# Kernel tuning notes

Hardware: AMD Instinct MI355X
Metric: run time of the kernel (lower is better)

## Reference

```python
import jax, jax.numpy as jnp
import numpy as np

B, S, D, H = 2, 2048, 2048, 16
HD = D // H            # 128
HALF = HD // 2         # 64
SOFTCAP = 50.0
ROPE_BASE = 10000.0


def setup_inputs() -> dict:
    key = jax.random.key(0)
    k1, k2, k3 = jax.random.split(key, 3)
    inputs = jax.random.normal(k1, (B, S, D), dtype=jnp.float32)
    # param init ~ nnx.initializers.normal() (stddev 0.01 default; scale to keep activations sane)
    w_in = jax.random.normal(k2, (D, H, 3 * HD), dtype=jnp.float32) * (1.0 / np.sqrt(D))
    w_out = jax.random.normal(k3, (H, HD, D), dtype=jnp.float32) * (1.0 / np.sqrt(D))
    # RoPE tables: [S, HALF]
    pos = jnp.arange(S, dtype=jnp.float32)[:, None]
    inv_freq = 1.0 / (ROPE_BASE ** (jnp.arange(HALF, dtype=jnp.float32) / HALF))
    ang = pos * inv_freq[None, :]
    rope_sin = jnp.sin(ang)
    rope_cos = jnp.cos(ang)
    # causal mask [1, 1, S, S]
    mask = jnp.tril(jnp.ones((S, S), dtype=bool))[None, None, :, :]
    return {"inputs": inputs, "w_in": w_in, "w_out": w_out,
            "rope_sin": rope_sin, "rope_cos": rope_cos, "mask": mask}


def apply_rope(x, sin, cos):
    # x: [B, S, H, HD]; sin/cos: [S, HALF] -> broadcast [1, S, 1, HALF]
    sin = sin[None, :, None, :]
    cos = cos[None, :, None, :]
    x1, x2 = x[..., :HALF], x[..., HALF:]
    return jnp.concatenate([x1 * cos - x2 * sin, x2 * cos + x1 * sin], axis=-1)


def reference(inputs, w_in, w_out, rope_sin, rope_cos, mask):
    dtype = inputs.dtype
    # fused QKV projection: [B, S, H, 3*HD]
    qkv = jnp.einsum('bsd,bhf->bshf'.replace('bhf', 'dhf'), inputs, w_in)
    q, k, v = jnp.split(qkv, 3, axis=-1)           # each [B, S, H, HD]
    q = apply_rope(q, rope_sin, rope_cos)
    k = apply_rope(k, rope_sin, rope_cos)
    q = q / jnp.sqrt(jnp.asarray(HD, dtype))
    scores = jnp.einsum('bqhd,bkhd->bhqk', q, k)   # [B, H, S, S]
    big_neg = jnp.finfo(dtype).min
    scores = jnp.where(mask, scores, big_neg)
    scores = jnp.tanh(scores / SOFTCAP) * SOFTCAP  # softcap
    attn = jax.nn.softmax(scores, axis=-1)
    x = jnp.einsum('bhqk,bkhd->bqhd', attn, v)     # [B, S, H, HD]
    out = jnp.einsum('bqhd,hdm->bqm', x, w_out)    # [B, S, D]
    return out
```

## Files before the change

### kernel.cpp

```cpp
#include <hip/hip_runtime.h>

#define B_ 2
#define S_ 2048
#define D_ 2048
#define H_ 16
#define HD_ 128
#define NT_ (S_ / 64)

typedef unsigned short u16;
typedef __bf16 bf16x8 __attribute__((ext_vector_type(8)));
typedef float f32x4 __attribute__((ext_vector_type(4)));

__device__ __forceinline__ float bf2f(u16 u) {
  unsigned int x = ((unsigned int)u) << 16;
  return __builtin_bit_cast(float, x);
}
__device__ __forceinline__ u16 f2bf(float f) {
  unsigned int u = __builtin_bit_cast(unsigned int, f);
  u += 0x7fffu + ((u >> 16) & 1u);
  return (u16)(u >> 16);
}
__device__ __forceinline__ void async16(const void* g, void* l) {
  __builtin_amdgcn_global_load_lds((const __attribute__((address_space(1))) void*)g,
                                   (__attribute__((address_space(3))) void*)l, 16, 0, 0);
}
__device__ __forceinline__ float vexp2(float x) {
  float r;
  asm("v_exp_f32 %0, %1" : "=v"(r) : "v"(x));
  return r;
}
__device__ __forceinline__ float vrcp(float x) {
  float r;
  asm("v_rcp_f32 %0, %1" : "=v"(r) : "v"(x));
  return r;
}

__global__ __launch_bounds__(256) void conv_f32_bf16(const float* __restrict__ in,
                                                     u16* __restrict__ outp, int n) {
  int idx = (blockIdx.x * 256 + threadIdx.x) * 4;
  int stride = gridDim.x * 256 * 4;
  for (; idx < n; idx += stride) {
    float4 v = *(const float4*)(in + idx);
    ushort4 ov = make_ushort4(f2bf(v.x), f2bf(v.y), f2bf(v.z), f2bf(v.w));
    *(ushort4*)(outp + idx) = ov;
  }
}

__global__ __launch_bounds__(256) void transpose_conv(const float* __restrict__ in,
                                                      u16* __restrict__ outp, int R, int C) {
  __shared__ float tile[32][33];
  int c0 = blockIdx.x * 32, r0 = blockIdx.y * 32;
  int tx = threadIdx.x & 31, ty = threadIdx.x >> 5;
#pragma unroll
  for (int yy = 0; yy < 32; yy += 8)
    tile[ty + yy][tx] = in[(size_t)(r0 + ty + yy) * C + c0 + tx];
  __syncthreads();
#pragma unroll
  for (int yy = 0; yy < 32; yy += 8)
    outp[(size_t)(c0 + ty + yy) * R + r0 + tx] = f2bf(tile[tx][ty + yy]);
}

__global__ __launch_bounds__(256) void transpose_v(const u16* __restrict__ in,
                                                   u16* __restrict__ outp) {
  __shared__ u16 tile[32][33];
  int bhh = blockIdx.z;
  const u16* ip = in + (size_t)bhh * S_ * HD_;
  u16* op = outp + (size_t)bhh * HD_ * S_;
  int hd0 = blockIdx.x * 32, s0 = blockIdx.y * 32;
  int tx = threadIdx.x & 31, ty = threadIdx.x >> 5;
#pragma unroll
  for (int yy = 0; yy < 32; yy += 8)
    tile[ty + yy][tx] = ip[(size_t)(s0 + ty + yy) * HD_ + hd0 + tx];
  __syncthreads();
#pragma unroll
  for (int yy = 0; yy < 32; yy += 8)
    op[(size_t)(hd0 + ty + yy) * S_ + s0 + tx] = tile[tx][ty + yy];
}

__global__ __launch_bounds__(256) void rope_kernel(u16* __restrict__ Q, u16* __restrict__ Kk,
                                                   const float* __restrict__ rsin,
                                                   const float* __restrict__ rcos) {
  int t = blockIdx.x * 256 + threadIdx.x;
  u16* base = blockIdx.y ? Kk : Q;
  float scale = blockIdx.y ? 1.0f : 0.08838834764831845f;
  int row = t >> 3, seg = t & 7;
  int s = row & (S_ - 1);
  int i0 = seg * 8;
  u16* p = base + (size_t)row * HD_;
  alignas(16) u16 x1[8], x2[8], o1[8], o2[8];
  *(uint4*)x1 = *(const uint4*)(p + i0);
  *(uint4*)x2 = *(const uint4*)(p + 64 + i0);
  alignas(16) float sn[8], cs[8];
  *(float4*)sn = *(const float4*)(rsin + s * 64 + i0);
  *(float4*)(sn + 4) = *(const float4*)(rsin + s * 64 + i0 + 4);
  *(float4*)cs = *(const float4*)(rcos + s * 64 + i0);
  *(float4*)(cs + 4) = *(const float4*)(rcos + s * 64 + i0 + 4);
#pragma unroll
  for (int j = 0; j < 8; ++j) {
    float a = bf2f(x1[j]), bb = bf2f(x2[j]);
    o1[j] = f2bf((a * cs[j] - bb * sn[j]) * scale);
    o2[j] = f2bf((bb * cs[j] + a * sn[j]) * scale);
  }
  *(uint4*)(p + i0) = *(uint4*)o1;
  *(uint4*)(p + 64 + i0) = *(uint4*)o2;
}

template <int EPI>
__global__ __launch_bounds__(256) void gemm_bt(const u16* __restrict__ A, const u16* __restrict__ Bt,
                                               float* __restrict__ C, int M, int N, int K,
                                               u16* __restrict__ Qo, u16* __restrict__ Ko,
                                               u16* __restrict__ Vo) {
  __shared__ alignas(16) u16 lsA[128 * 32];
  __shared__ alignas(16) u16 lsB[128 * 32];
  const int tid = threadIdx.x;
  const int lane = tid & 63, wid = tid >> 6;
  const int g = lane >> 4, lr = lane & 15;
  const int wr = wid >> 1, wc = wid & 1;
  const int m0 = blockIdx.y * 128, n0 = blockIdx.x * 128;
  f32x4 acc[4][4] = {};
  const int nk = K >> 5;
  for (int kt = 0; kt < nk; ++kt) {
    const int k0 = kt << 5;
    __syncthreads();
#pragma unroll
    for (int p = 0; p < 2; ++p) {
      const int c = p * 256 + tid;
      const int row = c >> 2;
      const int wb = (c & 3) << 4;
      async16((const char*)(A + (size_t)(m0 + row) * K + k0) + wb, (char*)lsA + c * 16);
      async16((const char*)(Bt + (size_t)(n0 + row) * K + k0) + wb, (char*)lsB + c * 16);
    }
    __syncthreads();
    bf16x8 af[4], bfr[4];
#pragma unroll
    for (int i = 0; i < 4; ++i)
      af[i] = *(const bf16x8*)((const char*)lsA + (wr * 64 + i * 16 + lr) * 64 + g * 16);
#pragma unroll
    for (int j = 0; j < 4; ++j)
      bfr[j] = *(const bf16x8*)((const char*)lsB + (wc * 64 + j * 16 + lr) * 64 + g * 16);
#pragma unroll
    for (int i = 0; i < 4; ++i)
#pragma unroll
      for (int j = 0; j < 4; ++j)
        acc[i][j] = __builtin_amdgcn_mfma_f32_16x16x32_bf16(af[i], bfr[j], acc[i][j], 0, 0, 0);
  }
  if (EPI == 0) {
#pragma unroll
    for (int i = 0; i < 4; ++i)
#pragma unroll
      for (int j = 0; j < 4; ++j)
#pragma unroll
        for (int r = 0; r < 4; ++r) {
          int m = m0 + wr * 64 + i * 16 + 4 * g + r;
          int n = n0 + wc * 64 + j * 16 + lr;
          C[(size_t)m * N + n] = acc[i][j][r];
        }
  } else {
    const int t = blockIdx.x;
    const int part = t % 3, h = t / 3;
    u16* dst = (part == 0) ? Qo : (part == 1 ? Ko : Vo);
#pragma unroll
    for (int i = 0; i < 4; ++i)
#pragma unroll
      for (int j = 0; j < 4; ++j)
#pragma unroll
        for (int r = 0; r < 4; ++r) {
          int m = m0 + wr * 64 + i * 16 + 4 * g + r;
          int hd = wc * 64 + j * 16 + lr;
          int b = m >> 11, s = m & (S_ - 1);
          dst[((size_t)(b * H_ + h) * S_ + s) * HD_ + hd] = f2bf(acc[i][j][r]);
        }
  }
}

__global__ __launch_bounds__(256) void attn_fwd(const u16* __restrict__ Q, const u16* __restrict__ K,
                                                const u16* __restrict__ VT, u16* __restrict__ X) {
  const int bx = blockIdx.x;
  const int bh = blockIdx.y;
  const int tid = threadIdx.x;
  const int lane = tid & 63, wid = tid >> 6;
  const int g = lane >> 4, lr = lane & 15;

  __shared__ alignas(16) u16 lsK[2][64 * 128];
  __shared__ alignas(16) u16 lsV[2][128 * 64];
  __shared__ alignas(16) u16 lsP[4][16 * 72];

  const u16* Qp = Q + (size_t)bh * S_ * HD_;
  const u16* Kp = K + (size_t)bh * S_ * HD_;
  const u16* Vp = VT + (size_t)bh * HD_ * S_;
  u16* myP = lsP[wid];
  const int b = bh >> 4, h = bh & 15;

  const float c1 = -0.057707802f;
  const float c2 = -144.26950409f;

#pragma unroll 1
  for (int pass = 0; pass < 2; ++pass) {
    const int qt = pass ? bx : (NT_ - 1 - bx);
    const int qrow = qt * 64 + wid * 16 + lr;
    const int qbase = qt * 64 + wid * 16 + 4 * g;

    bf16x8 qf[4];
#pragma unroll
    for (int kc = 0; kc < 4; ++kc)
      qf[kc] = *(const bf16x8*)(Qp + (size_t)qrow * HD_ + kc * 32 + g * 8);

    f32x4 o[8] = {};
    float psum[4] = {0.f, 0.f, 0.f, 0.f};

#pragma unroll
    for (int p = 0; p < 4; ++p) {
      int c = p * 256 + tid;
      int rowk = c >> 4;
      int wsk = ((c & 15) << 4) ^ ((rowk & 7) << 4);
      async16((const char*)Kp + (((size_t)rowk) << 8) + wsk, (char*)lsK[0] + c * 16);
      int rowv = c >> 3;
      int wsv = ((c & 7) << 4) ^ ((rowv & 7) << 4);
      async16((const char*)Vp + (size_t)rowv * (S_ * 2) + wsv, (char*)lsV[0] + c * 16);
    }
    __syncthreads();

    int cur = 0;
    for (int kt = 0; kt <= qt; ++kt) {
      if (kt < qt) {
        const int nxt = kt + 1;
#pragma unroll
        for (int p = 0; p < 4; ++p) {
          int c = p * 256 + tid;
          int rowk = c >> 4;
          int wsk = ((c & 15) << 4) ^ ((rowk & 7) << 4);
          async16((const char*)Kp + (((size_t)(nxt * 64 + rowk)) << 8) + wsk,
                  (char*)lsK[cur ^ 1] + c * 16);
          int rowv = c >> 3;
          int wsv = ((c & 7) << 4) ^ ((rowv & 7) << 4);
          async16((const char*)Vp + (size_t)rowv * (S_ * 2) + nxt * 128 + wsv,
                  (char*)lsV[cur ^ 1] + c * 16);
        }
      }
      f32x4 sc[4];
#pragma unroll
      for (int jn = 0; jn < 4; ++jn) {
        f32x4 a = {0.f, 0.f, 0.f, 0.f};
        const int row = jn * 16 + lr;
        const int sw = (row & 7) << 4;
#pragma unroll
        for (int kc = 0; kc < 4; ++kc) {
          int w = (kc * 64 + g * 16) ^ sw;
          bf16x8 kf = *(const bf16x8*)((const char*)lsK[cur] + row * 256 + w);
          a = __builtin_amdgcn_mfma_f32_16x16x32_bf16(qf[kc], kf, a, 0, 0, 0);
        }
        sc[jn] = a;
      }
#pragma unroll
      for (int jn = 0; jn < 4; ++jn) {
        int key = kt * 64 + jn * 16 + lr;
#pragma unroll
        for (int r = 0; r < 4; ++r) {
          float z = vexp2(c1 * sc[jn][r]);
          float p = vexp2(c2 * z * vrcp(1.f + z));
          if (key > qbase + r) p = 0.f;
          psum[r] += p;
          myP[(4 * g + r) * 72 + jn * 16 + lr] = f2bf(p);
        }
      }
#pragma unroll
      for (int kc = 0; kc < 2; ++kc) {
        bf16x8 pa = *(const bf16x8*)(myP + lr * 72 + kc * 32 + g * 8);
#pragma unroll
        for (int jh = 0; jh < 8; ++jh) {
          int row = jh * 16 + lr;
          int w = (kc * 64 + g * 16) ^ ((row & 7) << 4);
          bf16x8 vf = *(const bf16x8*)((const char*)lsV[cur] + row * 128 + w);
          o[jh] = __builtin_amdgcn_mfma_f32_16x16x32_bf16(pa, vf, o[jh], 0, 0, 0);
        }
      }
      __syncthreads();
      cur ^= 1;
    }
    float lsum[4];
#pragma unroll
    for (int r = 0; r < 4; ++r) {
      float s = psum[r];
#pragma unroll
      for (int msk = 1; msk < 16; msk <<= 1) s += __shfl_xor(s, msk, 64);
      lsum[r] = s;
    }
#pragma unroll
    for (int r = 0; r < 4; ++r) {
      float inv = 1.f / lsum[r];
      int s = qbase + r;
      u16* xp = X + ((size_t)(b * S_ + s)) * D_ + h * HD_;
#pragma unroll
      for (int jh = 0; jh < 8; ++jh) xp[jh * 16 + lr] = f2bf(o[jh][r] * inv);
    }
  }
}

extern "C" void kernel_launch(void* const* d_in, const int* in_sizes, int n_in,
                              void* d_out, int out_size, void* d_ws, size_t ws_size,
                              hipStream_t stream) {
  const float* inputs = (const float*)d_in[0];
  const float* w_in = (const float*)d_in[1];
  const float* w_out = (const float*)d_in[2];
  const float* rsin = (const float*)d_in[3];
  const float* rcos = (const float*)d_in[4];
  float* out = (float*)d_out;

  char* ws = (char*)d_ws;
  u16* bfA = (u16*)(ws);
  u16* w_inT = (u16*)(ws + 16777216);
  u16* Qraw = (u16*)(ws + 41943040);
  u16* Kraw = (u16*)(ws + 58720256);
  u16* Vraw = (u16*)(ws + 75497472);
  u16* VT = (u16*)(ws + 92274688);
  u16* Xbuf = (u16*)(ws);
  u16* w_outT = (u16*)(ws + 16777216);

  conv_f32_bf16<<<2048, 256, 0, stream>>>(inputs, bfA, B_ * S_ * D_);
  transpose_conv<<<dim3(6144 / 32, 2048 / 32), 256, 0, stream>>>(w_in, w_inT, 2048, 6144);
  gemm_bt<1><<<dim3(48, 32), 256, 0, stream>>>(bfA, w_inT, nullptr, 4096, 6144, 2048,
                                               Qraw, Kraw, Vraw);
  transpose_conv<<<dim3(2048 / 32, 2048 / 32), 256, 0, stream>>>(w_out, w_outT, 2048, 2048);
  rope_kernel<<<dim3(2048, 2), 256, 0, stream>>>(Qraw, Kraw, rsin, rcos);
  transpose_v<<<dim3(4, 64, 32), 256, 0, stream>>>(Vraw, VT);
  attn_fwd<<<dim3(NT_ / 2, 32), 256, 0, stream>>>(Qraw, Kraw, VT, Xbuf);
  gemm_bt<0><<<dim3(16, 32), 256, 0, stream>>>(Xbuf, w_outT, out, 4096, 2048, 2048,
                                               nullptr, nullptr, nullptr);
}
```

Measured before the change: 319.5 us.

## Rewrite GEMM with 6-stage async LDS pipeline, swizzled LDS, 256x128 tiles

Replaces the single-buffered 128x128 GEMM with a 512-thread 256x128 tile kernel. It keeps five K-tiles in flight through a six-buffer ring of async global-to-LDS loads, with XOR-swizzled LDS addressing to avoid bank conflicts. It also remaps workgroups with a grid swizzle for cache locality and raises wave priority around the MFMA block. The goal is to hide global load latency that the old per-iteration double sync exposed. In exchange it uses much more LDS (about 147KB), which caps occupancy at one block per CU, and it relies on a hand-set vmcnt wait.

```diff
diff --git a/kernel.cpp b/kernel.cpp
--- a/kernel.cpp
+++ b/kernel.cpp
@@ -6,6 +6,7 @@
 #define H_ 16
 #define HD_ 128
 #define NT_ (S_ / 64)
+#define NBUF 6
 
 typedef unsigned short u16;
 typedef __bf16 bf16x8 __attribute__((ext_vector_type(8)));
@@ -106,44 +107,83 @@
 }
 
 template <int EPI>
-__global__ __launch_bounds__(256) void gemm_bt(const u16* __restrict__ A, const u16* __restrict__ Bt,
-                                               float* __restrict__ C, int M, int N, int K,
-                                               u16* __restrict__ Qo, u16* __restrict__ Ko,
-                                               u16* __restrict__ Vo) {
-  __shared__ alignas(16) u16 lsA[128 * 32];
-  __shared__ alignas(16) u16 lsB[128 * 32];
+__global__ __launch_bounds__(512, 1) void gemm8p(const u16* __restrict__ A,
+                                                 const u16* __restrict__ Bt,
+                                                 float* __restrict__ C, int K, int N, int gx,
+                                                 u16* __restrict__ Qo, u16* __restrict__ Ko,
+                                                 u16* __restrict__ Vo) {
+  __shared__ alignas(16) u16 lsA[NBUF][256 * 32];
+  __shared__ alignas(16) u16 lsB[NBUF][128 * 32];
   const int tid = threadIdx.x;
-  const int lane = tid & 63, wid = tid >> 6;
+  const int lane = tid & 63;
+  const int wid = tid >> 6;
   const int g = lane >> 4, lr = lane & 15;
-  const int wr = wid >> 1, wc = wid & 1;
-  const int m0 = blockIdx.y * 128, n0 = blockIdx.x * 128;
+  const int wm = wid >> 1, wn = wid & 1;
+
+  const int nwg = gx << 4;
+  const int bid = blockIdx.x;
+  const int swz = (bid & 7) * (nwg >> 3) + (bid >> 3);
+  const int m_idx = swz & 15, n_idx = swz >> 4;
+  const size_t m0 = (size_t)m_idx * 256, n0 = (size_t)n_idx * 128;
+
+  const int la0 = tid, la1 = 512 + tid;
+  const int rowA0 = la0 >> 2, slA0 = la0 & 3;
+  const int rowA1 = la1 >> 2, slA1 = la1 & 3;
+  const int rowB = tid >> 2, slB = tid & 3;
+  const u16* srcA0 = A + (m0 + rowA0) * K + ((slA0 ^ ((rowA0 >> 1) & 3)) << 3);
+  const u16* srcA1 = A + (m0 + rowA1) * K + ((slA1 ^ ((rowA1 >> 1) & 3)) << 3);
+  const u16* srcB = Bt + (n0 + rowB) * K + ((slB ^ ((rowB >> 1) & 3)) << 3);
+
+#define STAGE(t, bufi)                                          \
+  {                                                             \
+    const int koff = (t) << 5;                                  \
+    async16(srcA0 + koff, (char*)lsA[bufi] + la0 * 16);         \
+    async16(srcA1 + koff, (char*)lsA[bufi] + la1 * 16);         \
+    async16(srcB + koff, (char*)lsB[bufi] + tid * 16);          \
+  }
+
+  int ofsA[4], ofsB[4];
+#pragma unroll
+  for (int i = 0; i < 4; ++i) {
+    int ra = wm * 64 + i * 16 + lr;
+    ofsA[i] = ra * 64 + ((g ^ ((ra >> 1) & 3)) << 4);
+    int rb = wn * 64 + i * 16 + lr;
+    ofsB[i] = rb * 64 + ((g ^ ((rb >> 1) & 3)) << 4);
+  }
+
   f32x4 acc[4][4] = {};
   const int nk = K >> 5;
+
+#pragma unroll
+  for (int t = 0; t < NBUF - 1; ++t) STAGE(t, t);
+  asm volatile("s_waitcnt vmcnt(12)" ::: "memory");
+  __builtin_amdgcn_s_barrier();
+
+  int buf = 0;
+#pragma unroll 1
   for (int kt = 0; kt < nk; ++kt) {
-    const int k0 = kt << 5;
-    __syncthreads();
-#pragma unroll
-    for (int p = 0; p < 2; ++p) {
-      const int c = p * 256 + tid;
-      const int row = c >> 2;
-      const int wb = (c & 3) << 4;
-      async16((const char*)(A + (size_t)(m0 + row) * K + k0) + wb, (char*)lsA + c * 16);
-      async16((const char*)(Bt + (size_t)(n0 + row) * K + k0) + wb, (char*)lsB + c * 16);
-    }
-    __syncthreads();
     bf16x8 af[4], bfr[4];
 #pragma unroll
-    for (int i = 0; i < 4; ++i)
-      af[i] = *(const bf16x8*)((const char*)lsA + (wr * 64 + i * 16 + lr) * 64 + g * 16);
-#pragma unroll
-    for (int j = 0; j < 4; ++j)
-      bfr[j] = *(const bf16x8*)((const char*)lsB + (wc * 64 + j * 16 + lr) * 64 + g * 16);
+    for (int i = 0; i < 4; ++i) af[i] = *(const bf16x8*)((const char*)lsA[buf] + ofsA[i]);
+#pragma unroll
+    for (int j = 0; j < 4; ++j) bfr[j] = *(const bf16x8*)((const char*)lsB[buf] + ofsB[j]);
+    const int st = kt + NBUF - 1;
+    const int sbuf = buf == 0 ? NBUF - 1 : buf - 1;
+    if (st < nk) STAGE(st, sbuf);
+    __builtin_amdgcn_s_barrier();
+    __builtin_amdgcn_s_setprio(1);
 #pragma unroll
     for (int i = 0; i < 4; ++i)
 #pragma unroll
       for (int j = 0; j < 4; ++j)
         acc[i][j] = __builtin_amdgcn_mfma_f32_16x16x32_bf16(af[i], bfr[j], acc[i][j], 0, 0, 0);
-  }
+    __builtin_amdgcn_s_setprio(0);
+    asm volatile("s_waitcnt vmcnt(12)" ::: "memory");
+    __builtin_amdgcn_s_barrier();
+    buf = buf == NBUF - 1 ? 0 : buf + 1;
+  }
+#undef STAGE
+
   if (EPI == 0) {
 #pragma unroll
     for (int i = 0; i < 4; ++i)
@@ -151,13 +191,12 @@
       for (int j = 0; j < 4; ++j)
 #pragma unroll
         for (int r = 0; r < 4; ++r) {
-          int m = m0 + wr * 64 + i * 16 + 4 * g + r;
-          int n = n0 + wc * 64 + j * 16 + lr;
-          C[(size_t)m * N + n] = acc[i][j][r];
+          size_t m = m0 + wm * 64 + i * 16 + 4 * g + r;
+          size_t n = n0 + wn * 64 + j * 16 + lr;
+          C[m * N + n] = acc[i][j][r];
         }
   } else {
-    const int t = blockIdx.x;
-    const int part = t % 3, h = t / 3;
+    const int part = n_idx % 3, h = n_idx / 3;
     u16* dst = (part == 0) ? Qo : (part == 1 ? Ko : Vo);
 #pragma unroll
     for (int i = 0; i < 4; ++i)
@@ -165,8 +204,8 @@
       for (int j = 0; j < 4; ++j)
 #pragma unroll
         for (int r = 0; r < 4; ++r) {
-          int m = m0 + wr * 64 + i * 16 + 4 * g + r;
-          int hd = wc * 64 + j * 16 + lr;
+          int m = (int)m0 + wm * 64 + i * 16 + 4 * g + r;
+          int hd = wn * 64 + j * 16 + lr;
           int b = m >> 11, s = m & (S_ - 1);
           dst[((size_t)(b * H_ + h) * S_ + s) * HD_ + hd] = f2bf(acc[i][j][r]);
         }
@@ -318,12 +357,11 @@
 
   conv_f32_bf16<<<2048, 256, 0, stream>>>(inputs, bfA, B_ * S_ * D_);
   transpose_conv<<<dim3(6144 / 32, 2048 / 32), 256, 0, stream>>>(w_in, w_inT, 2048, 6144);
-  gemm_bt<1><<<dim3(48, 32), 256, 0, stream>>>(bfA, w_inT, nullptr, 4096, 6144, 2048,
-                                               Qraw, Kraw, Vraw);
+  gemm8p<1><<<768, 512, 0, stream>>>(bfA, w_inT, nullptr, 2048, 6144, 48, Qraw, Kraw, Vraw);
   transpose_conv<<<dim3(2048 / 32, 2048 / 32), 256, 0, stream>>>(w_out, w_outT, 2048, 2048);
   rope_kernel<<<dim3(2048, 2), 256, 0, stream>>>(Qraw, Kraw, rsin, rcos);
   transpose_v<<<dim3(4, 64, 32), 256, 0, stream>>>(Vraw, VT);
   attn_fwd<<<dim3(NT_ / 2, 32), 256, 0, stream>>>(Qraw, Kraw, VT, Xbuf);
-  gemm_bt<0><<<dim3(16, 32), 256, 0, stream>>>(Xbuf, w_outT, out, 4096, 2048, 2048,
-                                               nullptr, nullptr, nullptr);
-}
+  gemm8p<0><<<256, 512, 0, stream>>>(Xbuf, w_outT, out, 2048, 2048, 16,
+                                     nullptr, nullptr, nullptr);
+}
```

Measured after the change: 310.3 us. -2.9%, faster.
